# Optimization experiments

Hardware: AMD Instinct MI355X
Metric: run time of the kernel (lower is better)

## Reference

```python
import jax, jax.numpy as jnp
import numpy as np


def setup_inputs() -> dict:
    key = jax.random.key(0)
    k1, k2 = jax.random.split(key)
    B, L, K, D = 131072, 4, 1024, 128
    residual = jax.random.normal(k1, (B, D), dtype=jnp.float32)
    codebooks = jax.random.normal(k2, (L, K, D), dtype=jnp.float32) * 0.1
    return {"residual": residual, "codebooks": codebooks}


def reference(residual, codebooks):
    """Residual VQ: per level, nearest-codeword assignment, gather, subtract.

    residual:  [B, D]
    codebooks: [L, K, D]
    Returns (quantized [B, D], codes [B, L] int32).
    """

    def step(res, emb):
        # squared L2 distances: ||r||^2 + ||e||^2 - 2 r.e  -> [B, K]
        x2 = jnp.sum(res * res, axis=1, keepdims=True)
        e2 = jnp.sum(emb * emb, axis=1)
        scores = x2 + e2 - 2.0 * (res @ emb.T)
        idx = jnp.argmin(scores, axis=1)            # [B]
        q = emb[idx]                                # gather [B, D]
        return res - q, (q, idx)

    _, (qs, idxs) = jax.lax.scan(step, residual, codebooks)
    quantized = jnp.sum(qs, axis=0)                 # [B, D]
    codes = idxs.T                                  # [B, L]
    return quantized, codes
```

## Files before the change

### kernel.cpp

```cpp
#include <hip/hip_runtime.h>
#include <math.h>


#define D_DIM 128
#define K_CB  1024
#define L_LVL 4
#define LK    (L_LVL * K_CB)
#define LKD   (LK * D_DIM)
#define NT2   16
#define TILE_ELEMS 8192
#define MARGIN_P5 4.5e-4f

typedef __bf16 bf16x8 __attribute__((ext_vector_type(8)));
typedef float  f32x16 __attribute__((ext_vector_type(16)));

static __device__ __forceinline__ float mulr(float a, float b) {
    float p = a * b; asm volatile("" : "+v"(p)); return p;
}

__global__ void rvq_prep(const float* __restrict__ cb,
                         __bf16* __restrict__ hi, __bf16* __restrict__ lo,
                         float* __restrict__ e2p, unsigned* __restrict__ flagcnt) {
    int j = blockIdx.x * blockDim.x + threadIdx.x;
    if (j == 0) *flagcnt = 0;
    const int lane = j & 63, kk = (j >> 6) & 7, s = (j >> 9) & 1,
              t = (j >> 10) & 15, lv = j >> 14;
    const int row  = lv * K_CB + t * 64 + s * 32 + (lane & 31);
    const int elem = kk * 16 + (lane >> 5) * 8;
    const float* src = cb + (size_t)row * D_DIM + elem;
    float4 a = *(const float4*)src;
    float4 b = *(const float4*)(src + 4);
    float f[8] = {a.x, a.y, a.z, a.w, b.x, b.y, b.z, b.w};
    bf16x8 hv, lvv;
    #pragma unroll
    for (int e = 0; e < 8; ++e) {
        __bf16 h = (__bf16)f[e];
        hv[e]  = h;
        lvv[e] = (__bf16)(f[e] - (float)h);
    }
    *(bf16x8*)(hi + (size_t)j * 8) = hv;
    *(bf16x8*)(lo + (size_t)j * 8) = lvv;

    if (j < LK) {
        const float* ep = cb + (size_t)j * D_DIM;
        float r8[8];
        #pragma unroll
        for (int q = 0; q < 8; ++q) r8[q] = mulr(ep[q], ep[q]);
        #pragma unroll
        for (int bb = 1; bb < 16; ++bb)
            #pragma unroll
            for (int q = 0; q < 8; ++q) r8[q] += mulr(ep[bb * 8 + q], ep[bb * 8 + q]);
        e2p[j] = ((r8[0] + r8[1]) + (r8[2] + r8[3])) + ((r8[4] + r8[5]) + (r8[6] + r8[7]));
    }
}

static __device__ __forceinline__ void stage_tile(
    const __bf16* srcTile, __bf16* dst, int wave, int lane) {
    #pragma unroll
    for (int c = 0; c < 4; ++c) {
        const int it = wave * 4 + c;
        __builtin_amdgcn_global_load_lds(
            (const __attribute__((address_space(1))) void*)(srcTile + it * 512 + lane * 8),
            (__attribute__((address_space(3))) void*)(dst + it * 512), 16, 0, 0);
    }
}

#define MFMA(A, Bv, C) __builtin_amdgcn_mfma_f32_32x32x16_bf16(A, Bv, C, 0, 0, 0)

static __device__ __forceinline__ float pack5(float sc, unsigned pk5) {
    unsigned u = __float_as_uint(sc);
    return __uint_as_float(((u + 16u) & ~31u) | pk5);
}

__global__ __launch_bounds__(256, 3)
void rvq_mfma(const float* __restrict__ residual,
              const float* __restrict__ codebooks,
              const __bf16* __restrict__ cbh, const __bf16* __restrict__ cbl,
              const float* __restrict__ e2p,
              unsigned* __restrict__ flagcnt, unsigned* __restrict__ flaglist,
              unsigned flagcap, float* __restrict__ out, int B) {
    __shared__ __align__(16) __bf16 bufh[2][TILE_ELEMS];
    __shared__ float e2s[K_CB];
    __shared__ int   bidxs[L_LVL][128];
    __shared__ unsigned char flg[128];

    const int tid  = threadIdx.x;
    const int wave = tid >> 6;
    const int lane = tid & 63;
    const int col  = lane & 31;
    const int h    = lane >> 5;
    const int rb   = wave * 32;
    const int grow = blockIdx.x * 128 + rb + col;

    if (tid < 128) flg[tid] = 0;

    bf16x8 Ah[8], Al[8];
    {
        const float* rowp = residual + (size_t)grow * D_DIM;
        #pragma unroll
        for (int kk = 0; kk < 8; ++kk) {
            const int d0 = kk * 16 + h * 8;
            float4 a = *(const float4*)(rowp + d0);
            float4 b = *(const float4*)(rowp + d0 + 4);
            float f[8] = {a.x, a.y, a.z, a.w, b.x, b.y, b.z, b.w};
            #pragma unroll
            for (int e = 0; e < 8; ++e) {
                __bf16 hh = (__bf16)f[e];
                Ah[kk][e] = hh;
                Al[kk][e] = (__bf16)(f[e] - (float)hh);
            }
        }
    }

    for (int l = 0; l < L_LVL; ++l) {
        const __bf16* cbhL = cbh + (size_t)l * NT2 * TILE_ELEMS;
        const __bf16* cblL = cbl + (size_t)l * NT2 * TILE_ELEMS;

        ((float4*)e2s)[tid] = ((const float4*)(e2p + l * K_CB))[tid];
        asm volatile("s_waitcnt vmcnt(0)" ::: "memory");

        float rbest[16], rbest2[16];
        #pragma unroll
        for (int s = 0; s < 16; ++s) { rbest[s] = 0.f; rbest2[s] = 0.f; }

        stage_tile(cbhL + 0 * TILE_ELEMS, &bufh[0][0], wave, lane);
        stage_tile(cbhL + 1 * TILE_ELEMS, &bufh[1][0], wave, lane);

        for (int t = 0; t < NT2; ++t) {
            const int cur = t & 1;
            const __bf16* bh  = &bufh[cur][0];
            const __bf16* blT = cblL + (size_t)t * TILE_ELEMS;

            if (t == 0) asm volatile("s_waitcnt vmcnt(4) lgkmcnt(0)" ::: "memory");
            __builtin_amdgcn_s_barrier();
            __builtin_amdgcn_sched_barrier(0);

            bf16x8 Blr[8];
            #pragma unroll
            for (int kk = 0; kk < 8; ++kk)
                Blr[kk] = *(const bf16x8*)(blT + kk * 512 + lane * 8);

            const float e2i0 = fmaf(-0.5f, e2s[t * 64 + col], 16.f);
            const float e2i1 = fmaf(-0.5f, e2s[t * 64 + 32 + col], 16.f);
            f32x16 acc0, acc1;
            #pragma unroll
            for (int s = 0; s < 16; ++s) { acc0[s] = e2i0; acc1[s] = e2i1; }

            __builtin_amdgcn_s_setprio(1);
            #pragma unroll
            for (int kk = 0; kk < 8; ++kk) {
                bf16x8 Bh0 = *(const bf16x8*)(bh + kk * 512 + lane * 8);
                bf16x8 Bh1 = *(const bf16x8*)(bh + 4096 + kk * 512 + lane * 8);
                acc0 = MFMA(Ah[kk], Bh0, acc0);
                acc0 = MFMA(Al[kk], Bh0, acc0);
                acc1 = MFMA(Ah[kk], Bh1, acc1);
                acc1 = MFMA(Al[kk], Bh1, acc1);
            }
            asm volatile("s_waitcnt vmcnt(0)" ::: "memory");
            __builtin_amdgcn_sched_barrier(0);
            #pragma unroll
            for (int kk = 0; kk < 8; ++kk) acc0 = MFMA(Ah[kk], Blr[kk], acc0);
            __builtin_amdgcn_s_setprio(0);

            #pragma unroll
            for (int kk = 0; kk < 8; ++kk)
                Blr[kk] = *(const bf16x8*)(blT + 4096 + kk * 512 + lane * 8);

            __builtin_amdgcn_sched_barrier(0);
            __builtin_amdgcn_s_barrier();
            asm volatile("" ::: "memory");
            if (t + 2 < NT2)
                stage_tile(cbhL + (size_t)(t + 2) * TILE_ELEMS, &bufh[cur][0], wave, lane);

            const unsigned pk0 = 31u - (unsigned)(t * 2);
            #pragma unroll
            for (int s = 0; s < 16; ++s) {
                float p0 = pack5(acc0[s], pk0);
                rbest2[s] = __builtin_amdgcn_fmed3f(p0, rbest[s], rbest2[s]);
                rbest[s]  = fmaxf(rbest[s], p0);
            }

            if (t + 2 < NT2) asm volatile("s_waitcnt vmcnt(4)" ::: "memory");
            else             asm volatile("s_waitcnt vmcnt(0)" ::: "memory");
            __builtin_amdgcn_sched_barrier(0);
            __builtin_amdgcn_s_setprio(1);
            #pragma unroll
            for (int kk = 0; kk < 8; ++kk) acc1 = MFMA(Ah[kk], Blr[kk], acc1);
            __builtin_amdgcn_s_setprio(0);

            const unsigned pk1 = 31u - (unsigned)(t * 2 + 1);
            #pragma unroll
            for (int s = 0; s < 16; ++s) {
                float p1 = pack5(acc1[s], pk1);
                rbest2[s] = __builtin_amdgcn_fmed3f(p1, rbest[s], rbest2[s]);
                rbest[s]  = fmaxf(rbest[s], p1);
            }
        }

        #pragma unroll
        for (int s = 0; s < 16; ++s) {
            float b = rbest[s], b2 = rbest2[s];
            int   c = col;
            #pragma unroll
            for (int m = 1; m <= 16; m <<= 1) {
                float bo  = __shfl_xor(b,  m, 64);
                float b2o = __shfl_xor(b2, m, 64);
                int   co  = __shfl_xor(c,  m, 64);
                float nb2 = fmaxf(fminf(b, bo), fmaxf(b2, b2o));
                if (bo > b || (bo == b && co < c)) { b = bo; c = co; }
                b2 = nb2;
            }
            const int rloc = (s & 3) + 8 * (s >> 2) + 4 * h;
            if (col == 0) {
                int idx5 = 31 - (int)(__float_as_uint(b) & 31u);
                bidxs[l][rb + rloc] = idx5 * 32 + c;
                if (b - b2 <= MARGIN_P5) flg[rb + rloc] = 1;
            }
        }
        __syncthreads();

        {
            const int bi = bidxs[l][rb + col];
            const float* qp = codebooks + ((size_t)l * K_CB + bi) * D_DIM;
            #pragma unroll
            for (int kk = 0; kk < 8; ++kk) {
                const int d0 = kk * 16 + h * 8;
                float4 qa = *(const float4*)(qp + d0);
                float4 qb = *(const float4*)(qp + d0 + 4);
                float q[8] = {qa.x, qa.y, qa.z, qa.w, qb.x, qb.y, qb.z, qb.w};
                #pragma unroll
                for (int e = 0; e < 8; ++e) {
                    float r = ((float)Ah[kk][e] + (float)Al[kk][e]) - q[e];
                    __bf16 hh = (__bf16)r;
                    Ah[kk][e] = hh;
                    Al[kk][e] = (__bf16)(r - (float)hh);
                }
            }
        }
    }

    {
        const float* rowp = residual + (size_t)grow * D_DIM;
        float* op = out + (size_t)grow * D_DIM;
        #pragma unroll
        for (int kk = 0; kk < 8; ++kk) {
            const int d0 = kk * 16 + h * 8;
            float4 a = *(const float4*)(rowp + d0);
            float4 b = *(const float4*)(rowp + d0 + 4);
            float f[8] = {a.x, a.y, a.z, a.w, b.x, b.y, b.z, b.w};
            float o[8];
            #pragma unroll
            for (int e = 0; e < 8; ++e)
                o[e] = f[e] - ((float)Ah[kk][e] + (float)Al[kk][e]);
            *(float4*)(op + d0)     = make_float4(o[0], o[1], o[2], o[3]);
            *(float4*)(op + d0 + 4) = make_float4(o[4], o[5], o[6], o[7]);
        }
    }
    if (tid < 128) {
        int row = blockIdx.x * 128 + tid;
        float4* cp = (float4*)(out + (size_t)B * D_DIM + (size_t)row * L_LVL);
        *cp = make_float4((float)bidxs[0][tid], (float)bidxs[1][tid],
                          (float)bidxs[2][tid], (float)bidxs[3][tid]);
        if (flg[tid]) {
            unsigned pos = atomicAdd(flagcnt, 1u);
            if (pos < flagcap) flaglist[pos] = row;
        }
    }
}

__global__ __launch_bounds__(256, 1)
void rvq_fixup(const float* __restrict__ residual,
               const float* __restrict__ codebooks,
               const float* __restrict__ e2p,
               const unsigned* __restrict__ flagcnt,
               const unsigned* __restrict__ flaglist,
               unsigned flagcap, float* __restrict__ out, int B) {
    __shared__ float rbuf[D_DIM];
    __shared__ float r0buf[D_DIM];
    __shared__ float x2s;
    __shared__ float redS[256];
    __shared__ int   redK[256];
    __shared__ int   codes_s[L_LVL];

    unsigned n = *flagcnt;
    if (n > flagcap) n = flagcap;

    for (unsigned b = blockIdx.x; b < n; b += gridDim.x) {
        int row = (int)flaglist[b];
        if (threadIdx.x < 32) {
            float4 v = ((const float4*)(residual + (size_t)row * D_DIM))[threadIdx.x];
            *(float4*)&rbuf[threadIdx.x * 4]  = v;
            *(float4*)&r0buf[threadIdx.x * 4] = v;
        }
        __syncthreads();

        for (int l = 0; l < L_LVL; ++l) {
            const float* cbl = codebooks + (size_t)l * K_CB * D_DIM;
            if (threadIdx.x == 0) {
                float r8[8];
                #pragma unroll
                for (int q = 0; q < 8; ++q) r8[q] = mulr(rbuf[q], rbuf[q]);
                for (int bb = 1; bb < 16; ++bb)
                    #pragma unroll
                    for (int q = 0; q < 8; ++q) r8[q] += mulr(rbuf[bb * 8 + q], rbuf[bb * 8 + q]);
                x2s = ((r8[0] + r8[1]) + (r8[2] + r8[3])) + ((r8[4] + r8[5]) + (r8[6] + r8[7]));
            }
            __syncthreads();
            float x2 = x2s;

            float bS = 3.4e38f;
            int   bK = 0x7fffffff;
            for (int m = 0; m < 4; ++m) {
                int k = threadIdx.x + m * 256;
                const float4* ek = (const float4*)(cbl + (size_t)k * D_DIM);
                double dd0 = 0.0, dd1 = 0.0, dd2 = 0.0, dd3 = 0.0;
                for (int c = 0; c < 32; c += 4) {
                    float4 v0 = ek[c], v1 = ek[c + 1], v2 = ek[c + 2], v3 = ek[c + 3];
                    dd0 = fma((double)v0.x, (double)rbuf[c * 4 + 0], dd0);
                    dd0 = fma((double)v0.y, (double)rbuf[c * 4 + 1], dd0);
                    dd0 = fma((double)v0.z, (double)rbuf[c * 4 + 2], dd0);
                    dd0 = fma((double)v0.w, (double)rbuf[c * 4 + 3], dd0);
                    dd1 = fma((double)v1.x, (double)rbuf[c * 4 + 4], dd1);
                    dd1 = fma((double)v1.y, (double)rbuf[c * 4 + 5], dd1);
                    dd1 = fma((double)v1.z, (double)rbuf[c * 4 + 6], dd1);
                    dd1 = fma((double)v1.w, (double)rbuf[c * 4 + 7], dd1);
                    dd2 = fma((double)v2.x, (double)rbuf[c * 4 + 8], dd2);
                    dd2 = fma((double)v2.y, (double)rbuf[c * 4 + 9], dd2);
                    dd2 = fma((double)v2.z, (double)rbuf[c * 4 + 10], dd2);
                    dd2 = fma((double)v2.w, (double)rbuf[c * 4 + 11], dd2);
                    dd3 = fma((double)v3.x, (double)rbuf[c * 4 + 12], dd3);
                    dd3 = fma((double)v3.y, (double)rbuf[c * 4 + 13], dd3);
                    dd3 = fma((double)v3.z, (double)rbuf[c * 4 + 14], dd3);
                    dd3 = fma((double)v3.w, (double)rbuf[c * 4 + 15], dd3);
                }
                float M = (float)((dd0 + dd1) + (dd2 + dd3));
                float A = x2 + e2p[l * K_CB + k];
                float S = A - 2.0f * M;
                if (S < bS || (S == bS && k < bK)) { bS = S; bK = k; }
            }
            redS[threadIdx.x] = bS; redK[threadIdx.x] = bK;
            __syncthreads();
            for (int s = 128; s > 0; s >>= 1) {
                if (threadIdx.x < (unsigned)s) {
                    float So = redS[threadIdx.x + s];
                    int   Ko = redK[threadIdx.x + s];
                    if (So < redS[threadIdx.x] ||
                        (So == redS[threadIdx.x] && Ko < redK[threadIdx.x])) {
                        redS[threadIdx.x] = So; redK[threadIdx.x] = Ko;
                    }
                }
                __syncthreads();
            }
            int bi = redK[0];
            if (threadIdx.x == 0) codes_s[l] = bi;
            if (threadIdx.x < 32) {
                float4 q = ((const float4*)(cbl + (size_t)bi * D_DIM))[threadIdx.x];
                float4* p = (float4*)&rbuf[threadIdx.x * 4];
                float4 x = *p;
                x.x -= q.x; x.y -= q.y; x.z -= q.z; x.w -= q.w;
                *p = x;
            }
            __syncthreads();
        }

        if (threadIdx.x < 32) {
            float4 a = *(float4*)&r0buf[threadIdx.x * 4];
            float4 r = *(float4*)&rbuf[threadIdx.x * 4];
            ((float4*)(out + (size_t)row * D_DIM))[threadIdx.x] =
                make_float4(a.x - r.x, a.y - r.y, a.z - r.z, a.w - r.w);
        }
        if (threadIdx.x == 0) {
            float4* cp = (float4*)(out + (size_t)B * D_DIM + (size_t)row * L_LVL);
            *cp = make_float4((float)codes_s[0], (float)codes_s[1],
                              (float)codes_s[2], (float)codes_s[3]);
        }
        __syncthreads();
    }
}

extern "C" void kernel_launch(void* const* d_in, const int* in_sizes, int n_in,
                              void* d_out, int out_size, void* d_ws, size_t ws_size,
                              hipStream_t stream) {
    const float* residual  = (const float*)d_in[0];
    const float* codebooks = (const float*)d_in[1];
    float* out = (float*)d_out;
    int B = in_sizes[0] / D_DIM;

    const size_t E2_BYTES = LK * sizeof(float);
    const size_t CB_BYTES = (size_t)LKD * 2;

    float*    e2p      = (float*)d_ws;
    __bf16*   cbh      = (__bf16*)((char*)d_ws + E2_BYTES);
    __bf16*   cblo     = (__bf16*)((char*)d_ws + E2_BYTES + CB_BYTES);
    unsigned* flagcnt  = (unsigned*)((char*)d_ws + E2_BYTES + 2 * CB_BYTES);
    unsigned* flaglist = flagcnt + 16;
    unsigned  flagcap  = (unsigned)((ws_size - (E2_BYTES + 2 * CB_BYTES + 64)) / 4);
    if (flagcap > (unsigned)B) flagcap = (unsigned)B;

    hipLaunchKernelGGL(rvq_prep, dim3(LKD / 8 / 256), dim3(256), 0, stream,
                       codebooks, cbh, cblo, e2p, flagcnt);
    hipLaunchKernelGGL(rvq_mfma, dim3(B / 128), dim3(256), 0, stream,
                       residual, codebooks, cbh, cblo, e2p,
                       flagcnt, flaglist, flagcap, out, B);
    hipLaunchKernelGGL(rvq_fixup, dim3(1024), dim3(256), 0, stream,
                       residual, codebooks, e2p, flagcnt, flaglist, flagcap, out, B);
}
```

Before: 764.6 us.

## Triple-buffer LDS codebook tiles and prefetch both low-part halves early

```diff
diff --git a/kernel.cpp b/kernel.cpp
--- a/kernel.cpp
+++ b/kernel.cpp
@@ -72,14 +72,14 @@
     return __uint_as_float(((u + 16u) & ~31u) | pk5);
 }
 
-__global__ __launch_bounds__(256, 3)
+__global__ __launch_bounds__(256)
 void rvq_mfma(const float* __restrict__ residual,
               const float* __restrict__ codebooks,
               const __bf16* __restrict__ cbh, const __bf16* __restrict__ cbl,
               const float* __restrict__ e2p,
               unsigned* __restrict__ flagcnt, unsigned* __restrict__ flaglist,
               unsigned flagcap, float* __restrict__ out, int B) {
-    __shared__ __align__(16) __bf16 bufh[2][TILE_ELEMS];
+    __shared__ __align__(16) __bf16 bufh[3][TILE_ELEMS];
     __shared__ float e2s[K_CB];
     __shared__ int   bidxs[L_LVL][128];
     __shared__ unsigned char flg[128];
@@ -127,18 +127,24 @@
         stage_tile(cbhL + 1 * TILE_ELEMS, &bufh[1][0], wave, lane);
 
         for (int t = 0; t < NT2; ++t) {
-            const int cur = t & 1;
-            const __bf16* bh  = &bufh[cur][0];
+            const __bf16* bh  = &bufh[t % 3][0];
             const __bf16* blT = cblL + (size_t)t * TILE_ELEMS;
-
-            if (t == 0) asm volatile("s_waitcnt vmcnt(4) lgkmcnt(0)" ::: "memory");
+            const bool haveStage = (t + 2 < NT2);
+
+            if (t == 0) asm volatile("s_waitcnt vmcnt(0) lgkmcnt(0)" ::: "memory");
             __builtin_amdgcn_s_barrier();
             __builtin_amdgcn_sched_barrier(0);
 
-            bf16x8 Blr[8];
+            bf16x8 Bl0[8], Bl1[8];
             #pragma unroll
             for (int kk = 0; kk < 8; ++kk)
-                Blr[kk] = *(const bf16x8*)(blT + kk * 512 + lane * 8);
+                Bl0[kk] = *(const bf16x8*)(blT + kk * 512 + lane * 8);
+            #pragma unroll
+            for (int kk = 0; kk < 8; ++kk)
+                Bl1[kk] = *(const bf16x8*)(blT + 4096 + kk * 512 + lane * 8);
+            if (haveStage)
+                stage_tile(cbhL + (size_t)(t + 2) * TILE_ELEMS,
+                           &bufh[(t + 2) % 3][0], wave, lane);
 
             const float e2i0 = fmaf(-0.5f, e2s[t * 64 + col], 16.f);
             const float e2i1 = fmaf(-0.5f, e2s[t * 64 + 32 + col], 16.f);
@@ -156,21 +162,15 @@
                 acc1 = MFMA(Ah[kk], Bh1, acc1);
                 acc1 = MFMA(Al[kk], Bh1, acc1);
             }
-            asm volatile("s_waitcnt vmcnt(0)" ::: "memory");
+            __builtin_amdgcn_s_setprio(0);
+
+            if (haveStage) asm volatile("s_waitcnt vmcnt(20)" ::: "memory");
+            else           asm volatile("s_waitcnt vmcnt(16)" ::: "memory");
             __builtin_amdgcn_sched_barrier(0);
-            #pragma unroll
-            for (int kk = 0; kk < 8; ++kk) acc0 = MFMA(Ah[kk], Blr[kk], acc0);
+            __builtin_amdgcn_s_setprio(1);
+            #pragma unroll
+            for (int kk = 0; kk < 8; ++kk) acc0 = MFMA(Ah[kk], Bl0[kk], acc0);
             __builtin_amdgcn_s_setprio(0);
-
-            #pragma unroll
-            for (int kk = 0; kk < 8; ++kk)
-                Blr[kk] = *(const bf16x8*)(blT + 4096 + kk * 512 + lane * 8);
-
-            __builtin_amdgcn_sched_barrier(0);
-            __builtin_amdgcn_s_barrier();
-            asm volatile("" ::: "memory");
-            if (t + 2 < NT2)
-                stage_tile(cbhL + (size_t)(t + 2) * TILE_ELEMS, &bufh[cur][0], wave, lane);
 
             const unsigned pk0 = 31u - (unsigned)(t * 2);
             #pragma unroll
@@ -180,12 +180,12 @@
                 rbest[s]  = fmaxf(rbest[s], p0);
             }
 
-            if (t + 2 < NT2) asm volatile("s_waitcnt vmcnt(4)" ::: "memory");
-            else             asm volatile("s_waitcnt vmcnt(0)" ::: "memory");
+            if (haveStage) asm volatile("s_waitcnt vmcnt(4)" ::: "memory");
+            else           asm volatile("s_waitcnt vmcnt(0)" ::: "memory");
             __builtin_amdgcn_sched_barrier(0);
             __builtin_amdgcn_s_setprio(1);
             #pragma unroll
-            for (int kk = 0; kk < 8; ++kk) acc1 = MFMA(Ah[kk], Blr[kk], acc1);
+            for (int kk = 0; kk < 8; ++kk) acc1 = MFMA(Ah[kk], Bl1[kk], acc1);
             __builtin_amdgcn_s_setprio(0);
 
             const unsigned pk1 = 31u - (unsigned)(t * 2 + 1);
```

Result: faster. 705.9 us (-7.7%).

## Prune fixup candidates with bf16 pre-scan and per-level error bound

Applied to the files above, without the earlier changes.

```diff
diff --git a/kernel.cpp b/kernel.cpp
--- a/kernel.cpp
+++ b/kernel.cpp
@@ -22,7 +22,6 @@
                          __bf16* __restrict__ hi, __bf16* __restrict__ lo,
                          float* __restrict__ e2p, unsigned* __restrict__ flagcnt) {
     int j = blockIdx.x * blockDim.x + threadIdx.x;
-    if (j == 0) *flagcnt = 0;
     const int lane = j & 63, kk = (j >> 6) & 7, s = (j >> 9) & 1,
               t = (j >> 10) & 15, lv = j >> 14;
     const int row  = lv * K_CB + t * 64 + s * 32 + (lane & 31);
@@ -51,6 +50,16 @@
             #pragma unroll
             for (int q = 0; q < 8; ++q) r8[q] += mulr(ep[bb * 8 + q], ep[bb * 8 + q]);
         e2p[j] = ((r8[0] + r8[1]) + (r8[2] + r8[3])) + ((r8[4] + r8[5]) + (r8[6] + r8[7]));
+
+        float lsum = 0.f;
+        for (int q2 = 0; q2 < D_DIM; ++q2) {
+            float v = ep[q2];
+            __bf16 hh = (__bf16)v;
+            float dl = v - (float)hh;
+            lsum = fmaf(dl, dl, lsum);
+        }
+        unsigned* elmaxu = flagcnt + 4;
+        atomicMax(&elmaxu[j >> 10], __float_as_uint(sqrtf(lsum)));
     }
 }
 
@@ -72,7 +81,7 @@
     return __uint_as_float(((u + 16u) & ~31u) | pk5);
 }
 
-__global__ __launch_bounds__(256, 3)
+__global__ __launch_bounds__(256)
 void rvq_mfma(const float* __restrict__ residual,
               const float* __restrict__ codebooks,
               const __bf16* __restrict__ cbh, const __bf16* __restrict__ cbl,
@@ -271,17 +280,19 @@
 __global__ __launch_bounds__(256, 1)
 void rvq_fixup(const float* __restrict__ residual,
                const float* __restrict__ codebooks,
+               const __bf16* __restrict__ cbh,
                const float* __restrict__ e2p,
                const unsigned* __restrict__ flagcnt,
                const unsigned* __restrict__ flaglist,
                unsigned flagcap, float* __restrict__ out, int B) {
     __shared__ float rbuf[D_DIM];
     __shared__ float r0buf[D_DIM];
-    __shared__ float x2s;
+    __shared__ float x2s, smins;
     __shared__ float redS[256];
     __shared__ int   redK[256];
     __shared__ int   codes_s[L_LVL];
 
+    const float* elmax = (const float*)(flagcnt + 4);
     unsigned n = *flagcnt;
     if (n > flagcap) n = flagcap;
 
@@ -296,6 +307,7 @@
 
         for (int l = 0; l < L_LVL; ++l) {
             const float* cbl = codebooks + (size_t)l * K_CB * D_DIM;
+            const __bf16* cbhL = cbh + (size_t)l * NT2 * TILE_ELEMS;
             if (threadIdx.x == 0) {
                 float r8[8];
                 #pragma unroll
@@ -308,9 +320,49 @@
             __syncthreads();
             float x2 = x2s;
 
+            float s4[4];
+            float sm = 3.4e38f;
+            #pragma unroll
+            for (int m = 0; m < 4; ++m) {
+                int k = threadIdx.x + m * 256;
+                int t = k >> 6, s = (k >> 5) & 1, c = k & 31;
+                const __bf16* kb = cbhL + t * 8192 + s * 4096 + c * 8;
+                float c0 = 0.f, c1 = 0.f, c2 = 0.f, c3 = 0.f;
+                #pragma unroll
+                for (int kk = 0; kk < 8; ++kk) {
+                    bf16x8 a  = *(const bf16x8*)(kb + kk * 512);
+                    bf16x8 bb = *(const bf16x8*)(kb + kk * 512 + 256);
+                    const float* rp = rbuf + kk * 16;
+                    c0 = fmaf((float)a[0], rp[0], c0);  c1 = fmaf((float)a[1], rp[1], c1);
+                    c2 = fmaf((float)a[2], rp[2], c2);  c3 = fmaf((float)a[3], rp[3], c3);
+                    c0 = fmaf((float)a[4], rp[4], c0);  c1 = fmaf((float)a[5], rp[5], c1);
+                    c2 = fmaf((float)a[6], rp[6], c2);  c3 = fmaf((float)a[7], rp[7], c3);
+                    c0 = fmaf((float)bb[0], rp[8], c0); c1 = fmaf((float)bb[1], rp[9], c1);
+                    c2 = fmaf((float)bb[2], rp[10], c2);c3 = fmaf((float)bb[3], rp[11], c3);
+                    c0 = fmaf((float)bb[4], rp[12], c0);c1 = fmaf((float)bb[5], rp[13], c1);
+                    c2 = fmaf((float)bb[6], rp[14], c2);c3 = fmaf((float)bb[7], rp[15], c3);
+                }
+                float Mh = (c0 + c1) + (c2 + c3);
+                float S = (x2 + e2p[l * K_CB + k]) - 2.0f * Mh;
+                s4[m] = S;
+                sm = fminf(sm, S);
+            }
+            redS[threadIdx.x] = sm;
+            __syncthreads();
+            for (int s = 128; s > 0; s >>= 1) {
+                if (threadIdx.x < (unsigned)s)
+                    redS[threadIdx.x] = fminf(redS[threadIdx.x], redS[threadIdx.x + s]);
+                __syncthreads();
+            }
+            if (threadIdx.x == 0) smins = redS[0];
+            __syncthreads();
+            const float thr = smins + 2.0f * (sqrtf(x2) * elmax[l] + 1e-4f);
+
             float bS = 3.4e38f;
             int   bK = 0x7fffffff;
+            #pragma unroll
             for (int m = 0; m < 4; ++m) {
+                if (s4[m] > thr) continue;
                 int k = threadIdx.x + m * 256;
                 const float4* ek = (const float4*)(cbl + (size_t)k * D_DIM);
                 double dd0 = 0.0, dd1 = 0.0, dd2 = 0.0, dd3 = 0.0;
@@ -397,11 +449,13 @@
     unsigned  flagcap  = (unsigned)((ws_size - (E2_BYTES + 2 * CB_BYTES + 64)) / 4);
     if (flagcap > (unsigned)B) flagcap = (unsigned)B;
 
+    hipMemsetAsync(flagcnt, 0, 32, stream);
     hipLaunchKernelGGL(rvq_prep, dim3(LKD / 8 / 256), dim3(256), 0, stream,
                        codebooks, cbh, cblo, e2p, flagcnt);
     hipLaunchKernelGGL(rvq_mfma, dim3(B / 128), dim3(256), 0, stream,
                        residual, codebooks, cbh, cblo, e2p,
                        flagcnt, flaglist, flagcap, out, B);
     hipLaunchKernelGGL(rvq_fixup, dim3(1024), dim3(256), 0, stream,
-                       residual, codebooks, e2p, flagcnt, flaglist, flagcap, out, B);
-}
+                       residual, codebooks, cbh, e2p,
+                       flagcnt, flaglist, flagcap, out, B);
+}
```

After: 638.7 us (median of 2 runs). 1.2x faster.
